# Kernel tuning notes

Measured on AMD Instinct MI355X. Metric: run time of the kernel, lower is better.

## Reference

```python
import jax, jax.numpy as jnp
import numpy as np

N, S, Q, P = 100000, 64, 50, 3  # pauli words, heads, qubits, pauli basis
EPS = 1e-12  # F.normalize clamp


def setup_inputs() -> dict:
    key = jax.random.key(0)
    k1, k2, k3, k4 = jax.random.split(key, 4)
    return {
        "batch_pauli_tensor": jax.random.uniform(k1, (N, Q, P), dtype=jnp.float32),
        "batch_coeff": jax.random.normal(k2, (N,), dtype=jnp.float32),
        "heads_param": jax.random.normal(k3, (S, Q, P), dtype=jnp.float32),
        "head_ratios_param": jax.random.normal(k4, (S,), dtype=jnp.float32),
    }


def reference(batch_pauli_tensor, batch_coeff, heads_param, head_ratios_param):
    s = heads_param.shape[0]
    heads = jax.nn.softplus(heads_param * 20.0)
    heads = heads / jnp.maximum(jnp.sum(heads, axis=-1, keepdims=True), EPS)
    hr = jax.nn.softplus(head_ratios_param * 20.0)
    hr = hr / jnp.maximum(jnp.sum(hr), EPS)
    hr = (hr + 0.001 / s) / 1.001
    # coverage: per-(word, head, qubit) match prob -> product over qubits -> ratio-weighted sum
    cov = jnp.einsum('nqp,sqp->nsq', batch_pauli_tensor, heads)  # [n, s, q]
    cov = jnp.prod(cov, axis=-1)                                 # [n, s]
    cov = jnp.einsum('s,ns->n', hr, cov)                         # [n]
    # variance loss
    return jnp.sum(batch_coeff ** 2 / cov)
```

## Files before the change

kernel.cpp:

```cpp
#include <hip/hip_runtime.h>
#include <math.h>

#define N_Q 50
#define N_P 3
#define N_S 64
#define ROW 150
#define ROWP 153
#define BLK_N 64
#define THREADS 256
#define SCHUNK 16

#define WS_HP_OFF 12544
#define WS_HRV_OFF 50944

__device__ __forceinline__ float softplus20(float x) {
    float z = x * 20.0f;
    return fmaxf(z, 0.0f) + log1pf(expf(-fabsf(z)));
}

__global__ void precompute_kernel(const float* __restrict__ heads_param,
                                  const float* __restrict__ hr_param,
                                  float* __restrict__ HP,
                                  float* __restrict__ hrv) {
    const int tid = threadIdx.x;

    if (tid < N_S) {
        float sp = softplus20(hr_param[tid]);
        float tot = sp;
        #pragma unroll
        for (int off = 32; off; off >>= 1) tot += __shfl_xor(tot, off);
        float hr = sp / fmaxf(tot, 1e-12f);
        hrv[tid] = (hr + 0.001f / (float)N_S) / 1.001f;
    }

    for (int idx = tid; idx < N_S * N_Q; idx += THREADS) {
        int q = idx / N_S;
        int s = idx - q * N_S;
        const float* hp = heads_param + ((size_t)s * N_Q + q) * N_P;
        float sp0 = softplus20(hp[0]);
        float sp1 = softplus20(hp[1]);
        float sp2 = softplus20(hp[2]);
        float denom = fmaxf(sp0 + sp1 + sp2, 1e-12f);
        float* o = HP + ((size_t)q * N_S + s) * 3;
        o[0] = sp0 / denom;
        o[1] = sp1 / denom;
        o[2] = sp2 / denom;
    }
}

__global__ __launch_bounds__(THREADS) void main_kernel(
    const float* __restrict__ A, const float* __restrict__ coeff,
    const float* __restrict__ HP, const float* __restrict__ hrv,
    double* __restrict__ partials, int N) {
    __shared__ float Atile[BLK_N * ROWP];
    __shared__ float covs[4][BLK_N];

    const int tid = threadIdx.x;
    const int lane = tid & 63;
    const int wave = tid >> 6;
    const int nbase = blockIdx.x * BLK_N;

    {
        const int nelem2 = BLK_N * (ROW / 2);
        for (int i = tid; i < nelem2; i += THREADS) {
            int row = i / (ROW / 2);
            int col2 = i - row * (ROW / 2);
            int n = nbase + row;
            if (n >= N) n = N - 1;
            const float2 v = *(const float2*)(A + (size_t)n * ROW + col2 * 2);
            const int la = row * ROWP + col2 * 2;
            Atile[la + 0] = v.x;
            Atile[la + 1] = v.y;
        }
    }
    __syncthreads();

    const int s0 = __builtin_amdgcn_readfirstlane(wave * SCHUNK);
    const float* __restrict__ Hw = HP + s0 * 3;

    float prod[SCHUNK];
    #pragma unroll
    for (int i = 0; i < SCHUNK; ++i) prod[i] = 1.0f;

    const float* Arow = Atile + lane * ROWP;

    #pragma unroll 2
    for (int q = 0; q < N_Q; ++q) {
        float a0 = Arow[q * 3 + 0];
        float a1 = Arow[q * 3 + 1];
        float a2 = Arow[q * 3 + 2];
        const float* Hq = Hw + q * (N_S * 3);
        #pragma unroll
        for (int i = 0; i < SCHUNK; ++i) {
            float d = fmaf(Hq[3 * i + 0], a0,
                     fmaf(Hq[3 * i + 1], a1, Hq[3 * i + 2] * a2));
            prod[i] *= d;
        }
    }

    float acc = 0.0f;
    #pragma unroll
    for (int i = 0; i < SCHUNK; ++i) acc = fmaf(hrv[s0 + i], prod[i], acc);

    covs[wave][lane] = acc;
    __syncthreads();

    if (wave == 0) {
        const int n = nbase + lane;
        float cov = covs[0][lane] + covs[1][lane] + covs[2][lane] + covs[3][lane];
        float term = 0.0f;
        if (n < N) {
            float c = coeff[n];
            term = (c * c) / cov;
        }
        double td = (double)term;
        #pragma unroll
        for (int off = 32; off; off >>= 1) td += __shfl_down(td, off);
        if (lane == 0) partials[blockIdx.x] = td;
    }
}

__global__ void reduce_kernel(const double* __restrict__ partials, int num,
                              float* __restrict__ out) {
    __shared__ double red[4];
    double s = 0.0;
    for (int i = threadIdx.x; i < num; i += THREADS) s += partials[i];
    #pragma unroll
    for (int off = 32; off; off >>= 1) s += __shfl_down(s, off);
    const int wave = threadIdx.x >> 6;
    const int lane = threadIdx.x & 63;
    if (lane == 0) red[wave] = s;
    __syncthreads();
    if (threadIdx.x == 0) out[0] = (float)(red[0] + red[1] + red[2] + red[3]);
}

extern "C" void kernel_launch(void* const* d_in, const int* in_sizes, int n_in,
                              void* d_out, int out_size, void* d_ws, size_t ws_size,
                              hipStream_t stream) {
    const float* A           = (const float*)d_in[0];
    const float* coeff       = (const float*)d_in[1];
    const float* heads_param = (const float*)d_in[2];
    const float* hr_param    = (const float*)d_in[3];
    const int N = in_sizes[1];
    const int nblocks = (N + BLK_N - 1) / BLK_N;

    char* ws = (char*)d_ws;
    double* partials = (double*)ws;
    float* HP  = (float*)(ws + WS_HP_OFF);
    float* hrv = (float*)(ws + WS_HRV_OFF);
    float* out = (float*)d_out;

    precompute_kernel<<<1, THREADS, 0, stream>>>(heads_param, hr_param, HP, hrv);
    main_kernel<<<nblocks, THREADS, 0, stream>>>(A, coeff, HP, hrv, partials, N);
    reduce_kernel<<<1, THREADS, 0, stream>>>(partials, nblocks, out);
}
```

Baseline: 156.2 us.

## Double-buffer head weights in registers, fuse final reduction, parallelize precompute

The main loop now loads each qubit's head weights as float4 vectors into two register buffers, so the next qubit's loads are issued while the current one is being multiplied. The separate reduce kernel is removed: the last block to finish, detected with an atomic counter, sums the partials, which saves one launch. The precompute kernel is spread over multiple blocks instead of one. The costs are more registers, which can lower occupancy, and per-lane (non-scalar) loads of head weights where the old code used uniform scalar loads.

```diff
diff --git a/kernel.cpp b/kernel.cpp
--- a/kernel.cpp
+++ b/kernel.cpp
@@ -10,8 +10,9 @@
 #define THREADS 256
 #define SCHUNK 16
 
-#define WS_HP_OFF 12544
-#define WS_HRV_OFF 50944
+#define WS_CNT_OFF 12544
+#define WS_HP_OFF 12608
+#define WS_HRV_OFF 51008
 
 __device__ __forceinline__ float softplus20(float x) {
     float z = x * 20.0f;
@@ -21,19 +22,24 @@
 __global__ void precompute_kernel(const float* __restrict__ heads_param,
                                   const float* __restrict__ hr_param,
                                   float* __restrict__ HP,
-                                  float* __restrict__ hrv) {
+                                  float* __restrict__ hrv,
+                                  int* __restrict__ cnt) {
     const int tid = threadIdx.x;
 
-    if (tid < N_S) {
-        float sp = softplus20(hr_param[tid]);
-        float tot = sp;
-        #pragma unroll
-        for (int off = 32; off; off >>= 1) tot += __shfl_xor(tot, off);
-        float hr = sp / fmaxf(tot, 1e-12f);
-        hrv[tid] = (hr + 0.001f / (float)N_S) / 1.001f;
+    if (blockIdx.x == 0) {
+        if (tid == 0) *cnt = 0;
+        if (tid < N_S) {
+            float sp = softplus20(hr_param[tid]);
+            float tot = sp;
+            #pragma unroll
+            for (int off = 32; off; off >>= 1) tot += __shfl_xor(tot, off);
+            float hr = sp / fmaxf(tot, 1e-12f);
+            hrv[tid] = (hr + 0.001f / (float)N_S) / 1.001f;
+        }
     }
 
-    for (int idx = tid; idx < N_S * N_Q; idx += THREADS) {
+    int idx = blockIdx.x * blockDim.x + tid;
+    if (idx < N_S * N_Q) {
         int q = idx / N_S;
         int s = idx - q * N_S;
         const float* hp = heads_param + ((size_t)s * N_Q + q) * N_P;
@@ -48,12 +54,32 @@
     }
 }
 
+__device__ __forceinline__ void loadH(float4 (&B)[12], const float4* __restrict__ p) {
+    #pragma unroll
+    for (int j = 0; j < 12; ++j) B[j] = p[j];
+}
+
+__device__ __forceinline__ void computeQ(const float4 (&B)[12],
+                                         float a0, float a1, float a2,
+                                         float (&p)[SCHUNK]) {
+    #pragma unroll
+    for (int g = 0; g < 4; ++g) {
+        float4 b0 = B[3 * g], b1 = B[3 * g + 1], b2 = B[3 * g + 2];
+        p[4 * g + 0] *= fmaf(b0.x, a0, fmaf(b0.y, a1, b0.z * a2));
+        p[4 * g + 1] *= fmaf(b0.w, a0, fmaf(b1.x, a1, b1.y * a2));
+        p[4 * g + 2] *= fmaf(b1.z, a0, fmaf(b1.w, a1, b2.x * a2));
+        p[4 * g + 3] *= fmaf(b2.y, a0, fmaf(b2.z, a1, b2.w * a2));
+    }
+}
+
 __global__ __launch_bounds__(THREADS) void main_kernel(
     const float* __restrict__ A, const float* __restrict__ coeff,
     const float* __restrict__ HP, const float* __restrict__ hrv,
-    double* __restrict__ partials, int N) {
+    double* __restrict__ partials, int* __restrict__ cnt,
+    float* __restrict__ out, int N) {
     __shared__ float Atile[BLK_N * ROWP];
     __shared__ float covs[4][BLK_N];
+    __shared__ int isLast;
 
     const int tid = threadIdx.x;
     const int lane = tid & 63;
@@ -75,8 +101,9 @@
     }
     __syncthreads();
 
-    const int s0 = __builtin_amdgcn_readfirstlane(wave * SCHUNK);
-    const float* __restrict__ Hw = HP + s0 * 3;
+    const int s0 = wave * SCHUNK;
+    const float4* __restrict__ Hbase =
+        (const float4*)HP + (size_t)wave * 12;
 
     float prod[SCHUNK];
     #pragma unroll
@@ -84,18 +111,22 @@
 
     const float* Arow = Atile + lane * ROWP;
 
-    #pragma unroll 2
-    for (int q = 0; q < N_Q; ++q) {
-        float a0 = Arow[q * 3 + 0];
-        float a1 = Arow[q * 3 + 1];
-        float a2 = Arow[q * 3 + 2];
-        const float* Hq = Hw + q * (N_S * 3);
-        #pragma unroll
-        for (int i = 0; i < SCHUNK; ++i) {
-            float d = fmaf(Hq[3 * i + 0], a0,
-                     fmaf(Hq[3 * i + 1], a1, Hq[3 * i + 2] * a2));
-            prod[i] *= d;
-        }
+    float4 B0[12], B1[12];
+    loadH(B0, Hbase);
+
+    for (int q = 0; q < N_Q; q += 2) {
+        loadH(B1, Hbase + (size_t)(q + 1) * 48);
+        float a0 = Arow[3 * q + 0];
+        float a1 = Arow[3 * q + 1];
+        float a2 = Arow[3 * q + 2];
+        computeQ(B0, a0, a1, a2, prod);
+        int qn = q + 2;
+        if (qn >= N_Q) qn = 0;
+        loadH(B0, Hbase + (size_t)qn * 48);
+        float c0 = Arow[3 * q + 3];
+        float c1 = Arow[3 * q + 4];
+        float c2 = Arow[3 * q + 5];
+        computeQ(B1, c0, c1, c2, prod);
     }
 
     float acc = 0.0f;
@@ -116,22 +147,26 @@
         double td = (double)term;
         #pragma unroll
         for (int off = 32; off; off >>= 1) td += __shfl_down(td, off);
-        if (lane == 0) partials[blockIdx.x] = td;
+        if (lane == 0) {
+            partials[blockIdx.x] = td;
+            __threadfence();
+            int v = atomicAdd(cnt, 1);
+            isLast = (v == (int)gridDim.x - 1);
+        }
     }
-}
+    __syncthreads();
 
-__global__ void reduce_kernel(const double* __restrict__ partials, int num,
-                              float* __restrict__ out) {
-    __shared__ double red[4];
-    double s = 0.0;
-    for (int i = threadIdx.x; i < num; i += THREADS) s += partials[i];
-    #pragma unroll
-    for (int off = 32; off; off >>= 1) s += __shfl_down(s, off);
-    const int wave = threadIdx.x >> 6;
-    const int lane = threadIdx.x & 63;
-    if (lane == 0) red[wave] = s;
-    __syncthreads();
-    if (threadIdx.x == 0) out[0] = (float)(red[0] + red[1] + red[2] + red[3]);
+    if (isLast) {
+        __threadfence();
+        double s = 0.0;
+        for (int i = tid; i < (int)gridDim.x; i += THREADS) s += partials[i];
+        #pragma unroll
+        for (int off = 32; off; off >>= 1) s += __shfl_down(s, off);
+        __shared__ double red[4];
+        if (lane == 0) red[wave] = s;
+        __syncthreads();
+        if (tid == 0) out[0] = (float)(red[0] + red[1] + red[2] + red[3]);
+    }
 }
 
 extern "C" void kernel_launch(void* const* d_in, const int* in_sizes, int n_in,
@@ -146,11 +181,14 @@
 
     char* ws = (char*)d_ws;
     double* partials = (double*)ws;
+    int*   cnt = (int*)(ws + WS_CNT_OFF);
     float* HP  = (float*)(ws + WS_HP_OFF);
     float* hrv = (float*)(ws + WS_HRV_OFF);
     float* out = (float*)d_out;
 
-    precompute_kernel<<<1, THREADS, 0, stream>>>(heads_param, hr_param, HP, hrv);
-    main_kernel<<<nblocks, THREADS, 0, stream>>>(A, coeff, HP, hrv, partials, N);
-    reduce_kernel<<<1, THREADS, 0, stream>>>(partials, nblocks, out);
+    const int pre_blocks = (N_S * N_Q + THREADS - 1) / THREADS;
+    precompute_kernel<<<pre_blocks, THREADS, 0, stream>>>(heads_param, hr_param,
+                                                          HP, hrv, cnt);
+    main_kernel<<<nblocks, THREADS, 0, stream>>>(A, coeff, HP, hrv, partials,
+                                                 cnt, out, N);
 }
```

Result: slower. 243.2 us (+55.7%).
